# Performance work log

Hardware: AMD Instinct MI355X
Metric: run time of the kernel (lower is better)

The kernel has to match this reference:

```python
import jax, jax.numpy as jnp
import numpy as np

B, L = 64, 512          # graphs, nodes per graph
N = B * L               # total nodes
INPUT_DIM, D, H, LAYERS, OUT = 128, 128, 8, 6, 10
DH = D // H
FF = 4 * D
E = 4 * N
SCALE = 0.02


def setup_inputs() -> dict:
    key = jax.random.key(0)
    ks = jax.random.split(key, 12)
    p = {}
    p['x'] = jax.random.normal(ks[0], (N, INPUT_DIM), jnp.float32)
    p['edge_index'] = jax.random.randint(ks[1], (2, E), 0, N, dtype=jnp.int64)
    p['batch'] = jnp.repeat(jnp.arange(B, dtype=jnp.int32), L)  # sorted graph ids
    p['max_nodes'] = L
    p['Wp'] = jax.random.normal(ks[2], (INPUT_DIM, D), jnp.float32) * SCALE
    p['bp'] = jnp.zeros((D,), jnp.float32)
    p['qkv_w'] = jax.random.normal(ks[3], (LAYERS, 3 * D, D), jnp.float32) * SCALE
    p['qkv_b'] = jnp.zeros((LAYERS, 3 * D), jnp.float32)
    p['out_w'] = jax.random.normal(ks[4], (LAYERS, D, D), jnp.float32) * SCALE
    p['out_b'] = jnp.zeros((LAYERS, D), jnp.float32)
    p['ln1_g'] = jnp.ones((LAYERS, D), jnp.float32)
    p['ln1_b'] = jnp.zeros((LAYERS, D), jnp.float32)
    p['ffn_w1'] = jax.random.normal(ks[5], (LAYERS, D, FF), jnp.float32) * SCALE
    p['ffn_b1'] = jnp.zeros((LAYERS, FF), jnp.float32)
    p['ffn_w2'] = jax.random.normal(ks[6], (LAYERS, FF, D), jnp.float32) * SCALE
    p['ffn_b2'] = jnp.zeros((LAYERS, D), jnp.float32)
    p['ln2_g'] = jnp.ones((LAYERS, D), jnp.float32)
    p['ln2_b'] = jnp.zeros((LAYERS, D), jnp.float32)
    p['cls_w1'] = jax.random.normal(ks[7], (D, D // 2), jnp.float32) * SCALE
    p['cls_b1'] = jnp.zeros((D // 2,), jnp.float32)
    p['cls_w2'] = jax.random.normal(ks[8], (D // 2, OUT), jnp.float32) * SCALE
    p['cls_b2'] = jnp.zeros((OUT,), jnp.float32)
    return p


def _ln(x, g, b, eps=1e-5):
    m = x.mean(-1, keepdims=True)
    v = ((x - m) ** 2).mean(-1, keepdims=True)
    return (x - m) * jax.lax.rsqrt(v + eps) * g + b


def _forward(x, batch, max_nodes, Wp, bp, qkv_w, qkv_b, out_w, out_b,
             ln1_g, ln1_b, ffn_w1, ffn_b1, ffn_w2, ffn_b2, ln2_g, ln2_b,
             cls_w1, cls_b1, cls_w2, cls_b2):
    n = x.shape[0]
    # --- vectorized ragged-to-dense (replaces the per-graph python loop) ---
    ones = jnp.ones((n,), jnp.int32)
    counts = jax.ops.segment_sum(ones, batch, num_segments=B)          # [B]
    starts = jnp.concatenate([jnp.zeros((1,), jnp.int32), jnp.cumsum(counts)[:-1]])
    pos = jnp.arange(n, dtype=jnp.int32) - starts[batch]               # slot within graph
    h0 = x @ Wp + bp                                                   # [N, D]
    h = jnp.zeros((B, max_nodes, D), h0.dtype).at[batch, pos].set(h0)  # [B, L, D]
    mask = jnp.zeros((B, max_nodes), bool).at[batch, pos].set(True)    # [B, L]
    # additive key-padding bias (src_key_padding_mask=~mask)
    bias = jnp.where(mask, 0.0, -1e9)[:, None, None, :]                # [B,1,1,L]
    inv_sqrt = 1.0 / np.sqrt(DH)
    for i in range(LAYERS):
        # --- post-norm MHA block ---
        qkv = jnp.einsum('bld,ed->ble', h, qkv_w[i]) + qkv_b[i]        # [B,L,3D]
        q, k, v = jnp.split(qkv, 3, axis=-1)
        q = q.reshape(B, max_nodes, H, DH).transpose(0, 2, 1, 3)       # [B,H,L,dh]
        k = k.reshape(B, max_nodes, H, DH).transpose(0, 2, 1, 3)
        v = v.reshape(B, max_nodes, H, DH).transpose(0, 2, 1, 3)
        scores = jnp.einsum('bhqd,bhkd->bhqk', q, k) * inv_sqrt + bias
        attn = jax.nn.softmax(scores, axis=-1)
        o = jnp.einsum('bhqk,bhkd->bhqd', attn, v)                     # [B,H,L,dh]
        o = o.transpose(0, 2, 1, 3).reshape(B, max_nodes, D)
        o = jnp.einsum('bld,ed->ble', o, out_w[i]) + out_b[i]
        h = _ln(h + o, ln1_g[i], ln1_b[i])
        # --- FFN block ---
        ff = jax.nn.relu(h @ ffn_w1[i] + ffn_b1[i]) @ ffn_w2[i] + ffn_b2[i]
        h = _ln(h + ff, ln2_g[i], ln2_b[i])
    # --- masked mean pooling per graph ---
    denom = jnp.maximum(counts.astype(h.dtype), 1.0)[:, None]          # [B,1]
    pooled = (h * mask[..., None].astype(h.dtype)).sum(axis=1) / denom # [B,D]
    # --- classifier head ---
    hid = jax.nn.relu(pooled @ cls_w1 + cls_b1)
    return hid @ cls_w2 + cls_b2                                       # [B,OUT]


def reference(x, edge_index, batch, max_nodes, Wp, bp, qkv_w, qkv_b, out_w, out_b,
              ln1_g, ln1_b, ffn_w1, ffn_b1, ffn_w2, ffn_b2, ln2_g, ln2_b,
              cls_w1, cls_b1, cls_w2, cls_b2):
    # edge_index is accepted (as in the torch module) but never used.
    return _forward(x, batch, max_nodes, Wp, bp, qkv_w, qkv_b, out_w, out_b,
                    ln1_g, ln1_b, ffn_w1, ffn_b1, ffn_w2, ffn_b2, ln2_g, ln2_b,
                    cls_w1, cls_b1, cls_w2, cls_b2)
```

## Files before the change

### kernel.cpp

```cpp
#include <hip/hip_runtime.h>
#include <hip/hip_bf16.h>


#define NROWS (64 * 512)
#define NLAYER 6

typedef __bf16 bf16x8 __attribute__((ext_vector_type(8)));
typedef float  f32x4  __attribute__((ext_vector_type(4)));
typedef float  f32x16 __attribute__((ext_vector_type(16)));

#define QSCALE 0.36067376022224085f

#if defined(__has_builtin)
#  if __has_builtin(__builtin_amdgcn_exp2f)
#    define FAST_EXP2(x) __builtin_amdgcn_exp2f(x)
#  endif
#endif
#ifndef FAST_EXP2
#  define FAST_EXP2(x) __expf((x) * 0.6931471805599453f)
#endif

__device__ __forceinline__ __hip_bfloat16 f2bf(float x) { return __float2bfloat16(x); }

__device__ __forceinline__ __hip_bfloat16 bf_rta(float a) {
  union { float f; unsigned u; } c{a};
  return __builtin_bit_cast(__hip_bfloat16, (unsigned short)((c.u + 0x8000u) >> 16));
}
__device__ __forceinline__ unsigned pk_rta(float a, float b) {
  union { float f; unsigned u; } ca{a}, cb{b};
  return ((ca.u + 0x8000u) >> 16) | ((cb.u + 0x8000u) & 0xFFFF0000u);
}

#define PN_X   (NROWS * 128)
#define PN_WP  (128 * 128)
#define PN_QW  (6 * 384 * 128)
#define PN_QB  (6 * 384)
#define PN_OW  (6 * 128 * 128)
#define PN_W1  (6 * 128 * 512)
#define PN_W2  (6 * 512 * 128)
#define PB1 PN_X
#define PB2 (PB1 + PN_WP)
#define PB3 (PB2 + PN_QW)
#define PB4 (PB3 + PN_QB)
#define PB5 (PB4 + PN_OW)
#define PB6 (PB5 + PN_W1)
#define PB7 (PB6 + PN_W2)

__global__ __launch_bounds__(256) void prep_kernel(
    const float* __restrict__ x, __hip_bfloat16* __restrict__ xb,
    const float* __restrict__ Wp, __hip_bfloat16* __restrict__ wp_t,
    const float* __restrict__ qkv_w, __hip_bfloat16* __restrict__ qkvw,
    const float* __restrict__ qkv_b, float* __restrict__ qb_s,
    const float* __restrict__ out_w, __hip_bfloat16* __restrict__ outw,
    const float* __restrict__ ffn_w1, __hip_bfloat16* __restrict__ w1t,
    const float* __restrict__ ffn_w2, __hip_bfloat16* __restrict__ w2t)
{
  const int idx = blockIdx.x * 256 + threadIdx.x;
  if (idx < PB1) {
    xb[idx] = f2bf(x[idx]);
  } else if (idx < PB2) {
    const int i = idx - PB1;
    const int c = i >> 7, r = i & 127;
    wp_t[i] = f2bf(Wp[r * 128 + c]);
  } else if (idx < PB3) {
    const int i = idx - PB2;
    const int row = (i >> 7) % 384;
    qkvw[i] = f2bf(qkv_w[i] * ((row < 128) ? QSCALE : 1.f));
  } else if (idx < PB4) {
    const int i = idx - PB3;
    qb_s[i] = qkv_b[i] * (((i % 384) < 128) ? QSCALE : 1.f);
  } else if (idx < PB5) {
    const int i = idx - PB4;
    outw[i] = f2bf(out_w[i]);
  } else if (idx < PB6) {
    const int i = idx - PB5;
    const int l = i >> 16, j = i & 65535;
    const int c = j >> 7, r = j & 127;
    w1t[i] = f2bf(ffn_w1[l * 65536 + r * 512 + c]);
  } else if (idx < PB7) {
    const int i = idx - PB6;
    const int l = i >> 16, j = i & 65535;
    const int c = j >> 9, r = j & 511;
    w2t[i] = f2bf(ffn_w2[l * 65536 + r * 128 + c]);
  }
}

__global__ __launch_bounds__(256) void gemm_fk(
    const __hip_bfloat16* __restrict__ A, const __hip_bfloat16* __restrict__ B,
    const float* __restrict__ bias, __hip_bfloat16* __restrict__ outb,
    __hip_bfloat16* __restrict__ hb,
    const float* __restrict__ lng, const float* __restrict__ lnb,
    int M, int K, int flags)
{
  __shared__ __align__(16) __hip_bfloat16 As[64 * 136];
  __shared__ __align__(16) __hip_bfloat16 Bs[128 * 136];

  const int tid = threadIdx.x;
  const int m0 = blockIdx.x << 6;
  const int wave = tid >> 6;
  const int lane = tid & 63;
  const int quad = lane >> 4;
  const int l15 = lane & 15;
  const int wrow = wave * 16;

  f32x4 acc[8];
#pragma unroll
  for (int ni = 0; ni < 8; ++ni) acc[ni] = (f32x4){0.f, 0.f, 0.f, 0.f};

  for (int kc = 0; kc < K; kc += 128) {
#pragma unroll
    for (int p = 0; p < 4; ++p) {
      const int e = tid + (p << 8);
      const int row = e >> 4;
      const int c = e & 15;
      *(uint4*)&As[row * 136 + c * 8] =
          *(const uint4*)(A + (size_t)(m0 + row) * K + kc + c * 8);
    }
#pragma unroll
    for (int p = 0; p < 8; ++p) {
      const int e = tid + (p << 8);
      const int row = e >> 4;
      const int c = e & 15;
      *(uint4*)&Bs[row * 136 + c * 8] =
          *(const uint4*)(B + (size_t)row * K + kc + c * 8);
    }
    __syncthreads();

#pragma unroll
    for (int ks = 0; ks < 4; ++ks) {
      const bf16x8 af = *(const bf16x8*)&As[(wrow + l15) * 136 + ks * 32 + quad * 8];
#pragma unroll
      for (int ni = 0; ni < 8; ++ni) {
        const bf16x8 bfr =
            *(const bf16x8*)&Bs[(ni * 16 + l15) * 136 + ks * 32 + quad * 8];
        acc[ni] = __builtin_amdgcn_mfma_f32_16x16x32_bf16(af, bfr, acc[ni], 0, 0, 0);
      }
    }
    if (kc + 128 < K) __syncthreads();
  }

  if (flags & 2) {
#pragma unroll
    for (int r = 0; r < 4; ++r) {
      const size_t row = (size_t)(m0 + wrow + quad * 4 + r);
      float s = 0.f, sq = 0.f;
#pragma unroll
      for (int ni = 0; ni < 8; ++ni) {
        const int cl = ni * 16 + l15;
        const float v = acc[ni][r] + bias[cl] +
                        __bfloat162float(hb[row * 128 + cl]);
        acc[ni][r] = v;
        s += v;
        sq += v * v;
      }
#pragma unroll
      for (int off = 1; off <= 8; off <<= 1) {
        s += __shfl_xor(s, off, 64);
        sq += __shfl_xor(sq, off, 64);
      }
      const float mean = s * (1.f / 128.f);
      const float var = sq * (1.f / 128.f) - mean * mean;
      const float rs = rsqrtf(var + 1e-5f);
#pragma unroll
      for (int ni = 0; ni < 8; ++ni) {
        const int cl = ni * 16 + l15;
        const float o = (acc[ni][r] - mean) * rs * lng[cl] + lnb[cl];
        hb[row * 128 + cl] = bf_rta(o);
      }
    }
  } else {
#pragma unroll
    for (int ni = 0; ni < 8; ++ni) {
      const int cl = ni * 16 + l15;
      const float bv = bias[cl];
#pragma unroll
      for (int r = 0; r < 4; ++r) {
        float v = acc[ni][r] + bv;
        if (flags & 1) v = fmaxf(v, 0.f);
        outb[(size_t)(m0 + wrow + quad * 4 + r) * 128 + cl] = bf_rta(v);
      }
    }
  }
}

__global__ __launch_bounds__(256) void gemm128T(
    const __hip_bfloat16* __restrict__ A, const __hip_bfloat16* __restrict__ B,
    const float* __restrict__ bias, __hip_bfloat16* __restrict__ outb,
    int M, int Nn, int K, int flags)
{
  __shared__ __align__(16) __hip_bfloat16 As[128 * 56];
  __shared__ __align__(16) __hip_bfloat16 Bs[128 * 56];

  const int tid = threadIdx.x;
  const int m0 = blockIdx.y << 7;
  const int n0 = blockIdx.x << 7;
  const int wave = tid >> 6;
  const int lane = tid & 63;
  const int wm = wave & 1;
  const int wn = wave >> 1;
  const int q = lane >> 4;
  const int l16 = lane & 15;

  f32x4 acc[4][4];
#pragma unroll
  for (int i = 0; i < 4; ++i)
#pragma unroll
    for (int j = 0; j < 4; ++j) acc[i][j] = (f32x4){0.f, 0.f, 0.f, 0.f};

  for (int k0 = 0; k0 < K; k0 += 32) {
#pragma unroll
    for (int p = 0; p < 2; ++p) {
      const int e = tid + (p << 8);
      const int row = e >> 2;
      const int c = e & 3;
      *(uint4*)&As[row * 56 + c * 8] =
          *(const uint4*)(A + (size_t)(m0 + row) * K + k0 + c * 8);
    }
#pragma unroll
    for (int p = 0; p < 2; ++p) {
      const int e = tid + (p << 8);
      const int row = e >> 2;
      const int c = e & 3;
      *(uint4*)&Bs[row * 56 + c * 8] =
          *(const uint4*)(B + (size_t)(n0 + row) * K + k0 + c * 8);
    }
    __syncthreads();

    bf16x8 af[4], bfr[4];
#pragma unroll
    for (int mi = 0; mi < 4; ++mi)
      af[mi] = *(const bf16x8*)&As[(wm * 64 + mi * 16 + l16) * 56 + q * 8];
#pragma unroll
    for (int ni = 0; ni < 4; ++ni)
      bfr[ni] = *(const bf16x8*)&Bs[(wn * 64 + ni * 16 + l16) * 56 + q * 8];
#pragma unroll
    for (int ni = 0; ni < 4; ++ni)
#pragma unroll
      for (int mi = 0; mi < 4; ++mi)
        acc[ni][mi] = __builtin_amdgcn_mfma_f32_16x16x32_bf16(
            bfr[ni], af[mi], acc[ni][mi], 0, 0, 0);
    if (k0 + 32 < K) __syncthreads();
  }

#pragma unroll
  for (int ni = 0; ni < 4; ++ni) {
    const int nf = n0 + wn * 64 + ni * 16;
    const f32x4 bv = *(const f32x4*)(bias + nf + q * 4);
#pragma unroll
    for (int mi = 0; mi < 4; ++mi) {
      const int node = m0 + wm * 64 + mi * 16 + l16;
      float v0 = acc[ni][mi][0] + bv[0];
      float v1 = acc[ni][mi][1] + bv[1];
      float v2 = acc[ni][mi][2] + bv[2];
      float v3 = acc[ni][mi][3] + bv[3];
      if (flags & 1) {
        v0 = fmaxf(v0, 0.f); v1 = fmaxf(v1, 0.f);
        v2 = fmaxf(v2, 0.f); v3 = fmaxf(v3, 0.f);
      }
      *(uint2*)(outb + (size_t)node * Nn + nf + q * 4) =
          make_uint2(pk_rta(v0, v1), pk_rta(v2, v3));
    }
  }
}

__global__ __launch_bounds__(512) void attn_kernel(
    const __hip_bfloat16* __restrict__ hbf,
    const __hip_bfloat16* __restrict__ qkvw_l,
    const float* __restrict__ qb_l,
    __hip_bfloat16* __restrict__ o)
{
  __shared__ __align__(16) __hip_bfloat16 Ks[512 * 24];
  __shared__ __align__(16) __hip_bfloat16 Vt[16 * 520];
  __shared__ __align__(16) __hip_bfloat16 PQ[8][1536];

  const int tid = threadIdx.x;
  const int b = blockIdx.x & 63;
  const int hh = blockIdx.x >> 6;
  const __hip_bfloat16* hrow = hbf + (size_t)b * 512 * 128;

  const int wave = tid >> 6;
  const int lane = tid & 63;
  const int l31 = lane & 31;
  const int l5 = lane >> 5;
  const int l15 = lane & 15;
  const int quad = lane >> 4;
  const int q0 = wave * 64;

  {
    f32x4 qacc[4], kacc[4], vacc[4];
#pragma unroll
    for (int mt = 0; mt < 4; ++mt) {
      qacc[mt] = (f32x4){0.f, 0.f, 0.f, 0.f};
      kacc[mt] = (f32x4){0.f, 0.f, 0.f, 0.f};
      vacc[mt] = (f32x4){0.f, 0.f, 0.f, 0.f};
    }
#pragma unroll
    for (int ks = 0; ks < 4; ++ks) {
      const int kc = ks * 32 + quad * 8;
      const bf16x8 wq = *(const bf16x8*)(qkvw_l + (size_t)(hh * 16 + l15) * 128 + kc);
      const bf16x8 wk = *(const bf16x8*)(qkvw_l + (size_t)(128 + hh * 16 + l15) * 128 + kc);
      const bf16x8 wv = *(const bf16x8*)(qkvw_l + (size_t)(256 + hh * 16 + l15) * 128 + kc);
#pragma unroll
      for (int mt = 0; mt < 4; ++mt) {
        const bf16x8 hf =
            *(const bf16x8*)(hrow + (size_t)(q0 + mt * 16 + l15) * 128 + kc);
        qacc[mt] = __builtin_amdgcn_mfma_f32_16x16x32_bf16(hf, wq, qacc[mt], 0, 0, 0);
        kacc[mt] = __builtin_amdgcn_mfma_f32_16x16x32_bf16(hf, wk, kacc[mt], 0, 0, 0);
        vacc[mt] = __builtin_amdgcn_mfma_f32_16x16x32_bf16(wv, hf, vacc[mt], 0, 0, 0);
      }
    }
    const float qb = qb_l[hh * 16 + l15];
    const float kb = qb_l[128 + hh * 16 + l15];
    const f32x4 vb = *(const f32x4*)(qb_l + 256 + hh * 16 + quad * 4);
#pragma unroll
    for (int mt = 0; mt < 4; ++mt)
#pragma unroll
      for (int r = 0; r < 4; ++r) {
        const int nd = mt * 16 + quad * 4 + r;
        PQ[wave][nd * 24 + l15] = bf_rta(qacc[mt][r] + qb);
        Ks[(q0 + nd) * 24 + l15] = bf_rta(kacc[mt][r] + kb);
        Vt[(quad * 4 + r) * 520 + q0 + mt * 16 + l15] = bf_rta(vacc[mt][r] + vb[r]);
      }
  }

  bf16x8 qf[2];
#pragma unroll
  for (int s = 0; s < 2; ++s)
    qf[s] = *(const bf16x8*)&PQ[wave][(s * 32 + l31) * 24 + l5 * 8];
  __syncthreads();

  __hip_bfloat16* Pw = &PQ[wave][0];
  const f32x16 z16 = {};
  f32x4 oacc[2][2];
#pragma unroll
  for (int s = 0; s < 2; ++s) { oacc[s][0] = (f32x4){0.f,0.f,0.f,0.f};
                                oacc[s][1] = (f32x4){0.f,0.f,0.f,0.f}; }
  float lacc[2] = {0.f, 0.f};

  for (int kt = 0; kt < 16; ++kt) {
    const bf16x8 kf = *(const bf16x8*)&Ks[(kt * 32 + l31) * 24 + l5 * 8];
    const bf16x8 vf = *(const bf16x8*)&Vt[l15 * 520 + kt * 32 + quad * 8];
#pragma unroll
    for (int s = 0; s < 2; ++s) {
      f32x16 st = __builtin_amdgcn_mfma_f32_32x32x16_bf16(kf, qf[s], z16, 0, 0, 0);
      float pr[16];
#pragma unroll
      for (int r = 0; r < 16; ++r) pr[r] = FAST_EXP2(st[r]);
      const float s0 = (pr[0] + pr[1]) + (pr[2] + pr[3]);
      const float s1 = (pr[4] + pr[5]) + (pr[6] + pr[7]);
      const float s2 = (pr[8] + pr[9]) + (pr[10] + pr[11]);
      const float s3 = (pr[12] + pr[13]) + (pr[14] + pr[15]);
      lacc[s] += (s0 + s1) + (s2 + s3);
#pragma unroll
      for (int g = 0; g < 4; ++g) {
        *(uint2*)&Pw[l31 * 40 + g * 8 + l5 * 4] =
            make_uint2(pk_rta(pr[g * 4 + 0], pr[g * 4 + 1]),
                       pk_rta(pr[g * 4 + 2], pr[g * 4 + 3]));
      }
#pragma unroll
      for (int g = 0; g < 2; ++g) {
        const bf16x8 pf = *(const bf16x8*)&Pw[(g * 16 + l15) * 40 + quad * 8];
        oacc[s][g] = __builtin_amdgcn_mfma_f32_16x16x32_bf16(vf, pf, oacc[s][g], 0, 0, 0);
      }
    }
  }

#pragma unroll
  for (int s = 0; s < 2; ++s) {
    const float lv = lacc[s] + __shfl_xor(lacc[s], 32, 64);
#pragma unroll
    for (int g = 0; g < 2; ++g) {
      const float lq = __shfl(lv, g * 16 + l15, 64);
      const float inv = 1.f / lq;
      const int qrow = q0 + s * 32 + g * 16 + l15;
      *(uint2*)(o + ((size_t)b * 512 + qrow) * 128 + hh * 16 + quad * 4) =
          make_uint2(pk_rta(oacc[s][g][0] * inv, oacc[s][g][1] * inv),
                     pk_rta(oacc[s][g][2] * inv, oacc[s][g][3] * inv));
    }
  }
}

__global__ __launch_bounds__(256) void head_kernel(
    const __hip_bfloat16* __restrict__ h,
    const float* __restrict__ w1, const float* __restrict__ b1,
    const float* __restrict__ w2, const float* __restrict__ b2,
    float* __restrict__ out)
{
  __shared__ float part[2][128];
  __shared__ float pooled[128];
  __shared__ float hid[64];

  const int b = blockIdx.x;
  const int tid = threadIdx.x;
  const int d = tid & 127;
  const int half = tid >> 7;

  const __hip_bfloat16* hp = h + ((size_t)b * 512 + (size_t)half * 256) * 128;
  float s = 0.f;
  for (int r = 0; r < 256; ++r) s += __bfloat162float(hp[(size_t)r * 128 + d]);
  part[half][d] = s;
  __syncthreads();

  if (tid < 128) pooled[tid] = (part[0][tid] + part[1][tid]) * (1.f / 512.f);
  __syncthreads();

  if (tid < 64) {
    float a = b1[tid];
    for (int dd = 0; dd < 128; ++dd) a = fmaf(pooled[dd], w1[dd * 64 + tid], a);
    hid[tid] = fmaxf(a, 0.f);
  }
  __syncthreads();

  if (tid < 10) {
    float a = b2[tid];
    for (int j = 0; j < 64; ++j) a = fmaf(hid[j], w2[j * 10 + tid], a);
    out[b * 10 + tid] = a;
  }
}

extern "C" void kernel_launch(void* const* d_in, const int* in_sizes, int n_in,
                              void* d_out, int out_size, void* d_ws, size_t ws_size,
                              hipStream_t stream)
{
  (void)in_sizes; (void)n_in; (void)out_size; (void)ws_size;

  const float* x      = (const float*)d_in[0];
  const float* Wp     = (const float*)d_in[4];
  const float* bp     = (const float*)d_in[5];
  const float* qkv_w  = (const float*)d_in[6];
  const float* qkv_b  = (const float*)d_in[7];
  const float* out_w  = (const float*)d_in[8];
  const float* out_b  = (const float*)d_in[9];
  const float* ln1_g  = (const float*)d_in[10];
  const float* ln1_b  = (const float*)d_in[11];
  const float* ffn_w1 = (const float*)d_in[12];
  const float* ffn_b1 = (const float*)d_in[13];
  const float* ffn_w2 = (const float*)d_in[14];
  const float* ffn_b2 = (const float*)d_in[15];
  const float* ln2_g  = (const float*)d_in[16];
  const float* ln2_b  = (const float*)d_in[17];
  const float* cw1    = (const float*)d_in[18];
  const float* cb1    = (const float*)d_in[19];
  const float* cw2    = (const float*)d_in[20];
  const float* cb2    = (const float*)d_in[21];

  const int N = NROWS;

  __hip_bfloat16* hbf   = (__hip_bfloat16*)d_ws;
  __hip_bfloat16* xb    = hbf + (size_t)N * 128;
  __hip_bfloat16* attnb = xb + (size_t)N * 128;
  __hip_bfloat16* ffb   = attnb + (size_t)N * 128;
  __hip_bfloat16* wp_t  = ffb + (size_t)N * 512;
  __hip_bfloat16* qkvw  = wp_t + 128 * 128;
  __hip_bfloat16* outw  = qkvw + 6 * 384 * 128;
  __hip_bfloat16* w1t   = outw + 6 * 128 * 128;
  __hip_bfloat16* w2t   = w1t + 6 * 512 * 128;
  float* qb_s = (float*)(w2t + 6 * 128 * 512);

  const dim3 blk(256);
  __hip_bfloat16* const nob = (__hip_bfloat16*)nullptr;
  const float* const nof = (const float*)nullptr;

  prep_kernel<<<dim3((PB7 + 255) / 256), blk, 0, stream>>>(
      x, xb, Wp, wp_t, qkv_w, qkvw, qkv_b, qb_s, out_w, outw,
      ffn_w1, w1t, ffn_w2, w2t);

  gemm_fk<<<dim3(N / 64), blk, 0, stream>>>(
      xb, wp_t, bp, hbf, nob, nof, nof, N, 128, 0);

  for (int i = 0; i < NLAYER; ++i) {
    attn_kernel<<<dim3(64 * 8), dim3(512), 0, stream>>>(
        hbf, qkvw + (size_t)i * 384 * 128, qb_s + (size_t)i * 384, attnb);

    gemm_fk<<<dim3(N / 64), blk, 0, stream>>>(
        attnb, outw + (size_t)i * 128 * 128, out_b + (size_t)i * 128,
        nob, hbf, ln1_g + (size_t)i * 128, ln1_b + (size_t)i * 128,
        N, 128, 2);

    gemm128T<<<dim3(4, N / 128), blk, 0, stream>>>(
        hbf, w1t + (size_t)i * 512 * 128, ffn_b1 + (size_t)i * 512,
        ffb, N, 512, 128, 1);

    gemm_fk<<<dim3(N / 64), blk, 0, stream>>>(
        ffb, w2t + (size_t)i * 128 * 512, ffn_b2 + (size_t)i * 128,
        nob, hbf, ln2_g + (size_t)i * 128, ln2_b + (size_t)i * 128,
        N, 512, 2);
  }

  head_kernel<<<dim3(64), blk, 0, stream>>>(hbf, cw1, cb1, cw2, cb2, (float*)d_out);
}
```

Before: 593.5 us.

## Fuse both FFN GEMMs, ReLU, residual and LayerNorm into one kernel

Replaces the separate up-projection GEMM and the down-projection+LayerNorm GEMM with a single kernel per 64-row tile. The 512-wide ReLU intermediate is produced 128 columns at a time into shared memory and consumed immediately by the second GEMM, so it is never written to or read from global memory. The cost is that every block reloads the full W1 and W2 weights through L2, that the kernel uses about 52 KB of shared memory per block (which limits occupancy), and that weight loads are not overlapped with compute.

```diff
diff --git a/kernel.cpp b/kernel.cpp
--- a/kernel.cpp
+++ b/kernel.cpp
@@ -183,82 +183,132 @@
   }
 }
 
-__global__ __launch_bounds__(256) void gemm128T(
-    const __hip_bfloat16* __restrict__ A, const __hip_bfloat16* __restrict__ B,
-    const float* __restrict__ bias, __hip_bfloat16* __restrict__ outb,
-    int M, int Nn, int K, int flags)
+__global__ __launch_bounds__(256) void ffn_fused(
+    __hip_bfloat16* __restrict__ hb,
+    const __hip_bfloat16* __restrict__ w1,
+    const __hip_bfloat16* __restrict__ w2,
+    const float* __restrict__ b1, const float* __restrict__ b2,
+    const float* __restrict__ lng, const float* __restrict__ lnb)
 {
-  __shared__ __align__(16) __hip_bfloat16 As[128 * 56];
-  __shared__ __align__(16) __hip_bfloat16 Bs[128 * 56];
+  __shared__ __align__(16) __hip_bfloat16 AF[64 * 136];
+  __shared__ __align__(16) __hip_bfloat16 Bs[128 * 136];
 
   const int tid = threadIdx.x;
-  const int m0 = blockIdx.y << 7;
-  const int n0 = blockIdx.x << 7;
+  const int m0 = blockIdx.x << 6;
   const int wave = tid >> 6;
   const int lane = tid & 63;
-  const int wm = wave & 1;
-  const int wn = wave >> 1;
-  const int q = lane >> 4;
-  const int l16 = lane & 15;
-
-  f32x4 acc[4][4];
-#pragma unroll
-  for (int i = 0; i < 4; ++i)
-#pragma unroll
-    for (int j = 0; j < 4; ++j) acc[i][j] = (f32x4){0.f, 0.f, 0.f, 0.f};
-
-  for (int k0 = 0; k0 < K; k0 += 32) {
-#pragma unroll
-    for (int p = 0; p < 2; ++p) {
+  const int quad = lane >> 4;
+  const int l15 = lane & 15;
+  const int wrow = wave * 16;
+
+#pragma unroll
+  for (int p = 0; p < 4; ++p) {
+    const int e = tid + (p << 8);
+    const int row = e >> 4, c = e & 15;
+    *(uint4*)&AF[row * 136 + c * 8] =
+        *(const uint4*)(hb + (size_t)(m0 + row) * 128 + c * 8);
+  }
+#pragma unroll
+  for (int p = 0; p < 8; ++p) {
+    const int e = tid + (p << 8);
+    const int row = e >> 4, c = e & 15;
+    *(uint4*)&Bs[row * 136 + c * 8] =
+        *(const uint4*)(w1 + (size_t)row * 128 + c * 8);
+  }
+  __syncthreads();
+
+  bf16x8 af[4];
+#pragma unroll
+  for (int ks = 0; ks < 4; ++ks)
+    af[ks] = *(const bf16x8*)&AF[(wrow + l15) * 136 + ks * 32 + quad * 8];
+
+  f32x4 oacc[8];
+#pragma unroll
+  for (int ni = 0; ni < 8; ++ni) oacc[ni] = (f32x4){0.f, 0.f, 0.f, 0.f};
+
+  for (int c = 0; c < 4; ++c) {
+    if (c > 0) {
+      __syncthreads();
+#pragma unroll
+      for (int p = 0; p < 8; ++p) {
+        const int e = tid + (p << 8);
+        const int row = e >> 4, cc = e & 15;
+        *(uint4*)&Bs[row * 136 + cc * 8] =
+            *(const uint4*)(w1 + (size_t)(c * 128 + row) * 128 + cc * 8);
+      }
+      __syncthreads();
+    }
+
+    f32x4 fc[8];
+#pragma unroll
+    for (int ni = 0; ni < 8; ++ni) fc[ni] = (f32x4){0.f, 0.f, 0.f, 0.f};
+#pragma unroll
+    for (int ks = 0; ks < 4; ++ks)
+#pragma unroll
+      for (int ni = 0; ni < 8; ++ni) {
+        const bf16x8 wf =
+            *(const bf16x8*)&Bs[(ni * 16 + l15) * 136 + ks * 32 + quad * 8];
+        fc[ni] = __builtin_amdgcn_mfma_f32_16x16x32_bf16(wf, af[ks], fc[ni], 0, 0, 0);
+      }
+#pragma unroll
+    for (int ni = 0; ni < 8; ++ni) {
+      const f32x4 bv = *(const f32x4*)(b1 + c * 128 + ni * 16 + quad * 4);
+      const float v0 = fmaxf(fc[ni][0] + bv[0], 0.f);
+      const float v1 = fmaxf(fc[ni][1] + bv[1], 0.f);
+      const float v2 = fmaxf(fc[ni][2] + bv[2], 0.f);
+      const float v3 = fmaxf(fc[ni][3] + bv[3], 0.f);
+      *(uint2*)&AF[(wrow + l15) * 136 + ni * 16 + quad * 4] =
+          make_uint2(pk_rta(v0, v1), pk_rta(v2, v3));
+    }
+    __syncthreads();
+
+#pragma unroll
+    for (int p = 0; p < 8; ++p) {
       const int e = tid + (p << 8);
-      const int row = e >> 2;
-      const int c = e & 3;
-      *(uint4*)&As[row * 56 + c * 8] =
-          *(const uint4*)(A + (size_t)(m0 + row) * K + k0 + c * 8);
-    }
-#pragma unroll
-    for (int p = 0; p < 2; ++p) {
-      const int e = tid + (p << 8);
-      const int row = e >> 2;
-      const int c = e & 3;
-      *(uint4*)&Bs[row * 56 + c * 8] =
-          *(const uint4*)(B + (size_t)(n0 + row) * K + k0 + c * 8);
+      const int row = e >> 4, cc = e & 15;
+      *(uint4*)&Bs[row * 136 + cc * 8] =
+          *(const uint4*)(w2 + (size_t)row * 512 + c * 128 + cc * 8);
     }
     __syncthreads();
 
-    bf16x8 af[4], bfr[4];
-#pragma unroll
-    for (int mi = 0; mi < 4; ++mi)
-      af[mi] = *(const bf16x8*)&As[(wm * 64 + mi * 16 + l16) * 56 + q * 8];
-#pragma unroll
-    for (int ni = 0; ni < 4; ++ni)
-      bfr[ni] = *(const bf16x8*)&Bs[(wn * 64 + ni * 16 + l16) * 56 + q * 8];
-#pragma unroll
-    for (int ni = 0; ni < 4; ++ni)
-#pragma unroll
-      for (int mi = 0; mi < 4; ++mi)
-        acc[ni][mi] = __builtin_amdgcn_mfma_f32_16x16x32_bf16(
-            bfr[ni], af[mi], acc[ni][mi], 0, 0, 0);
-    if (k0 + 32 < K) __syncthreads();
-  }
-
-#pragma unroll
-  for (int ni = 0; ni < 4; ++ni) {
-    const int nf = n0 + wn * 64 + ni * 16;
-    const f32x4 bv = *(const f32x4*)(bias + nf + q * 4);
-#pragma unroll
-    for (int mi = 0; mi < 4; ++mi) {
-      const int node = m0 + wm * 64 + mi * 16 + l16;
-      float v0 = acc[ni][mi][0] + bv[0];
-      float v1 = acc[ni][mi][1] + bv[1];
-      float v2 = acc[ni][mi][2] + bv[2];
-      float v3 = acc[ni][mi][3] + bv[3];
-      if (flags & 1) {
-        v0 = fmaxf(v0, 0.f); v1 = fmaxf(v1, 0.f);
-        v2 = fmaxf(v2, 0.f); v3 = fmaxf(v3, 0.f);
-      }
-      *(uint2*)(outb + (size_t)node * Nn + nf + q * 4) =
-          make_uint2(pk_rta(v0, v1), pk_rta(v2, v3));
+#pragma unroll
+    for (int ks2 = 0; ks2 < 4; ++ks2) {
+      const bf16x8 ff =
+          *(const bf16x8*)&AF[(wrow + l15) * 136 + ks2 * 32 + quad * 8];
+#pragma unroll
+      for (int ni = 0; ni < 8; ++ni) {
+        const bf16x8 wf =
+            *(const bf16x8*)&Bs[(ni * 16 + l15) * 136 + ks2 * 32 + quad * 8];
+        oacc[ni] = __builtin_amdgcn_mfma_f32_16x16x32_bf16(ff, wf, oacc[ni], 0, 0, 0);
+      }
+    }
+  }
+
+#pragma unroll
+  for (int r = 0; r < 4; ++r) {
+    const size_t row = (size_t)(m0 + wrow + quad * 4 + r);
+    float s = 0.f, sq = 0.f;
+#pragma unroll
+    for (int ni = 0; ni < 8; ++ni) {
+      const int cl = ni * 16 + l15;
+      const float v = oacc[ni][r] + b2[cl] + __bfloat162float(hb[row * 128 + cl]);
+      oacc[ni][r] = v;
+      s += v;
+      sq += v * v;
+    }
+#pragma unroll
+    for (int off = 1; off <= 8; off <<= 1) {
+      s += __shfl_xor(s, off, 64);
+      sq += __shfl_xor(sq, off, 64);
+    }
+    const float mean = s * (1.f / 128.f);
+    const float var = sq * (1.f / 128.f) - mean * mean;
+    const float rs = rsqrtf(var + 1e-5f);
+#pragma unroll
+    for (int ni = 0; ni < 8; ++ni) {
+      const int cl = ni * 16 + l15;
+      const float o = (oacc[ni][r] - mean) * rs * lng[cl] + lnb[cl];
+      hb[row * 128 + cl] = bf_rta(o);
     }
   }
 }
@@ -449,8 +499,7 @@
   __hip_bfloat16* hbf   = (__hip_bfloat16*)d_ws;
   __hip_bfloat16* xb    = hbf + (size_t)N * 128;
   __hip_bfloat16* attnb = xb + (size_t)N * 128;
-  __hip_bfloat16* ffb   = attnb + (size_t)N * 128;
-  __hip_bfloat16* wp_t  = ffb + (size_t)N * 512;
+  __hip_bfloat16* wp_t  = attnb + (size_t)N * 128;
   __hip_bfloat16* qkvw  = wp_t + 128 * 128;
   __hip_bfloat16* outw  = qkvw + 6 * 384 * 128;
   __hip_bfloat16* w1t   = outw + 6 * 128 * 128;
@@ -477,14 +526,10 @@
         nob, hbf, ln1_g + (size_t)i * 128, ln1_b + (size_t)i * 128,
         N, 128, 2);
 
-    gemm128T<<<dim3(4, N / 128), blk, 0, stream>>>(
-        hbf, w1t + (size_t)i * 512 * 128, ffn_b1 + (size_t)i * 512,
-        ffb, N, 512, 128, 1);
-
-    gemm_fk<<<dim3(N / 64), blk, 0, stream>>>(
-        ffb, w2t + (size_t)i * 128 * 512, ffn_b2 + (size_t)i * 128,
-        nob, hbf, ln2_g + (size_t)i * 128, ln2_b + (size_t)i * 128,
-        N, 512, 2);
+    ffn_fused<<<dim3(N / 64), blk, 0, stream>>>(
+        hbf, w1t + (size_t)i * 512 * 128, w2t + (size_t)i * 128 * 512,
+        ffn_b1 + (size_t)i * 512, ffn_b2 + (size_t)i * 128,
+        ln2_g + (size_t)i * 128, ln2_b + (size_t)i * 128);
   }
 
   head_kernel<<<dim3(64), blk, 0, stream>>>(hbf, cw1, cb1, cw2, cb2, (float*)d_out);
```

Result: faster. 511.8 us (-13.8%).
